# Optimization experiments

Hardware: AMD Instinct MI355X
Metric: run time of the kernel (lower is better)

## Reference

```python
import jax, jax.numpy as jnp
import numpy as np

ALPHA = 0.2  # LeakyReLU negative slope
NEG_INF = -9e15  # matches torch -9000000000000000.0


def setup_inputs() -> dict:
    key = jax.random.key(0)
    k1, k2, k3, k4, k5, k6 = jax.random.split(key, 6)
    N, F_in, F_out = 4096, 512, 256
    adj = jax.random.randint(k1, (N, N), 0, 2, dtype=jnp.int32)
    h = jax.random.normal(k2, (N, F_in), dtype=jnp.float32)
    # proj: Linear(F_in, F_out)
    W = jax.random.normal(k3, (F_in, F_out), dtype=jnp.float32) * (1.0 / np.sqrt(F_in))
    b = jax.random.normal(k4, (F_out,), dtype=jnp.float32) * 0.01
    # proj_a: Linear(2*F_out, 1) split into the two halves acting on src/dst features
    a1 = jax.random.normal(k5, (F_out,), dtype=jnp.float32) * (1.0 / np.sqrt(2 * F_out))
    a2 = jax.random.normal(k6, (F_out,), dtype=jnp.float32) * (1.0 / np.sqrt(2 * F_out))
    a_b = jnp.zeros((), dtype=jnp.float32)
    return {"adj": adj, "h": h, "W": W, "b": b, "a1": a1, "a2": a2, "a_b": a_b}


def reference(adj, h, W, b, a1, a2, a_b):
    # wh = proj(h): [N, F_out]
    wh = h @ W + b
    # Fused form of the N x N x 2F concat + Linear(2F,1):
    # logits[i, j] = wh[i] . a1 + wh[j] . a2 + a_b
    f_src = wh @ a1  # [N]
    f_dst = wh @ a2  # [N]
    e = jax.nn.leaky_relu(f_src[:, None] + f_dst[None, :] + a_b, negative_slope=ALPHA)
    e = jnp.where(adj > 0, e, NEG_INF)
    att = jax.nn.softmax(e, axis=-1)  # F.softmax legacy dim=1 for 2D
    # dropout: inference mode (no-op) for deterministic reference
    out = att @ wh  # [N, F_out]
    return jax.nn.elu(out)  # concat=True
```

## Files before the change

### kernel.cpp

```cpp
#include <hip/hip_runtime.h>

#define NN   4096
#define FIN  512
#define FOUT 256
#define ALPHA 0.2f

typedef __attribute__((ext_vector_type(8))) short short8;
typedef __attribute__((ext_vector_type(4))) float f32x4;
typedef unsigned short u16;
typedef unsigned int u32;
typedef unsigned long long u64;

__device__ __forceinline__ u16 f2bf(float x) {
    union { float f; unsigned u; } v; v.f = x;
    unsigned r = v.u + 0x7FFF + ((v.u >> 16) & 1);
    return (u16)(r >> 16);
}

__global__ __launch_bounds__(256) void k_wt(const float* __restrict__ W,
                                            u16* __restrict__ Wt,
                                            float* __restrict__ fs,
                                            float* __restrict__ fd) {
    __shared__ float s[64 * 65];
    const int t  = threadIdx.x;
    const int g  = (blockIdx.y * gridDim.x + blockIdx.x) * 256 + t;
    if (g < NN) fs[g] = 0.f; else fd[g - NN] = 0.f;
    const int f0 = blockIdx.x * 64;
    const int k0 = blockIdx.y * 64;
    #pragma unroll
    for (int p = 0; p < 4; ++p) {
        int q = t + 256 * p, rr = q >> 4, cc = q & 15;
        float4 w4 = *(const float4*)&W[(size_t)(k0 + rr) * FOUT + f0 + cc * 4];
        s[(cc * 4 + 0) * 65 + rr] = w4.x;
        s[(cc * 4 + 1) * 65 + rr] = w4.y;
        s[(cc * 4 + 2) * 65 + rr] = w4.z;
        s[(cc * 4 + 3) * 65 + rr] = w4.w;
    }
    __syncthreads();
    #pragma unroll
    for (int p = 0; p < 4; ++p) {
        int q = t + 256 * p, f = q >> 4, kg = q & 15;
        ushort4 o;
        o.x = f2bf(s[f * 65 + kg * 4 + 0]);
        o.y = f2bf(s[f * 65 + kg * 4 + 1]);
        o.z = f2bf(s[f * 65 + kg * 4 + 2]);
        o.w = f2bf(s[f * 65 + kg * 4 + 3]);
        *(ushort4*)&Wt[(size_t)(f0 + f) * FIN + k0 + kg * 4] = o;
    }
}

#define HS 520
__global__ __launch_bounds__(256) void k_pb(const float* __restrict__ h,
                                            const u16* __restrict__ Wt,
                                            const float* __restrict__ bias,
                                            const float* __restrict__ a1,
                                            const float* __restrict__ a2,
                                            const int* __restrict__ adj,
                                            u16* __restrict__ whT,
                                            float* __restrict__ fs,
                                            float* __restrict__ fd,
                                            u64* __restrict__ bits) {
    __shared__ u16 s_h[32 * HS];
    const int bid = blockIdx.x;
    const int t   = threadIdx.x;
    if (bid >= 512) {
        const int l = t & 63, wv = t >> 6;
        const int row  = (bid - 512) * 2 + (wv >> 1);
        const int half = wv & 1;
        const size_t base = (size_t)row * NN + half * 2048;
        u64* dst = bits + (size_t)row * 64 + half * 32;
        #pragma unroll
        for (int o = 0; o < 8; ++o) {
            u64 b0 = __ballot(adj[base + (o * 4 + 0) * 64 + l] > 0);
            u64 b1 = __ballot(adj[base + (o * 4 + 1) * 64 + l] > 0);
            u64 b2 = __ballot(adj[base + (o * 4 + 2) * 64 + l] > 0);
            u64 b3 = __ballot(adj[base + (o * 4 + 3) * 64 + l] > 0);
            if (l == 0) {
                dst[o * 4 + 0] = b0;
                dst[o * 4 + 1] = b1;
                dst[o * 4 + 2] = b2;
                dst[o * 4 + 3] = b3;
            }
        }
        return;
    }
    const int f0 = (bid & 3) * 64;
    const int i0 = (bid >> 2) * 32;
    #pragma unroll
    for (int p = 0; p < 16; ++p) {
        int q = t + 256 * p, row = q >> 7, c4 = q & 127;
        float4 v = *(const float4*)&h[(size_t)(i0 + row) * FIN + c4 * 4];
        ushort4 o; o.x = f2bf(v.x); o.y = f2bf(v.y); o.z = f2bf(v.z); o.w = f2bf(v.w);
        *(ushort4*)&s_h[row * HS + c4 * 4] = o;
    }
    __syncthreads();
    const int w = t >> 6, l = t & 63, n = l & 15, quad = l >> 4;
    const int hh = w & 1, fh = w >> 1;
    f32x4 acc[2] = {{0.f,0.f,0.f,0.f},{0.f,0.f,0.f,0.f}};
    #pragma unroll
    for (int k0 = 0; k0 < FIN; k0 += 32) {
        short8 a = *(const short8*)&s_h[(hh * 16 + n) * HS + k0 + quad * 8];
        short8 b0 = *(const short8*)&Wt[(size_t)(f0 + fh * 32 + n) * FIN + k0 + quad * 8];
        short8 b1 = *(const short8*)&Wt[(size_t)(f0 + fh * 32 + 16 + n) * FIN + k0 + quad * 8];
        acc[0] = __builtin_amdgcn_mfma_f32_16x16x32_bf16(a, b0, acc[0], 0, 0, 0);
        acc[1] = __builtin_amdgcn_mfma_f32_16x16x32_bf16(a, b1, acc[1], 0, 0, 0);
    }
    const int fb = f0 + fh * 32 + n;
    const float bv0 = bias[fb],  bv1 = bias[fb + 16];
    const float a10 = a1[fb],    a11 = a1[fb + 16];
    const float a20 = a2[fb],    a21 = a2[fb + 16];
    u16* wt_tile = whT + (size_t)(i0 >> 5) * (FOUT * 32);
    float d1[4], d2[4];
    #pragma unroll
    for (int r = 0; r < 4; ++r) {
        const int ic = hh * 16 + quad * 4 + r;
        const float v0 = acc[0][r] + bv0;
        const float v1 = acc[1][r] + bv1;
        wt_tile[fb * 32 + ic]        = f2bf(v0);
        wt_tile[(fb + 16) * 32 + ic] = f2bf(v1);
        d1[r] = v0 * a10 + v1 * a11;
        d2[r] = v0 * a20 + v1 * a21;
    }
    #pragma unroll
    for (int m = 1; m < 16; m <<= 1) {
        #pragma unroll
        for (int r = 0; r < 4; ++r) {
            d1[r] += __shfl_xor(d1[r], m);
            d2[r] += __shfl_xor(d2[r], m);
        }
    }
    if (n == 0) {
        #pragma unroll
        for (int r = 0; r < 4; ++r) {
            const int i = i0 + hh * 16 + quad * 4 + r;
            atomicAdd(&fs[i], d1[r]);
            atomicAdd(&fd[i], d2[r]);
        }
    }
}

#define BI 32
#define CJ 8

__device__ __forceinline__ void comp_step(
        const short8& b0, const short8& b1, const short8& b2, const short8& b3,
        const float* s_F, const float* s_H, int joff, int jq8,
        u32 w0, u32 w1, float E0, float G0, float E1, float G1,
        f32x4 (&acc)[2][4], float& rs0, float& rs1) {
    const float4 Fa = *(const float4*)&s_F[joff + jq8];
    const float4 Fb = *(const float4*)&s_F[joff + jq8 + 4];
    const float4 Ha = *(const float4*)&s_H[joff + jq8];
    const float4 Hb = *(const float4*)&s_H[joff + jq8 + 4];
    const u32 bw0 = w0 >> jq8, bw1 = w1 >> jq8;
    float q0, q1, q2, q3, q4, q5, q6, q7;
    u32 d0, d1, d2, d3;
    union { short8 v; u32 d[4]; } o0, o1;
#define PEL1(FV, HV, BW, K, E, G, RS, PP) do { \
        float _m = fmaxf((E) * (FV), (G) * (HV)); \
        PP = ((BW) & (1u << (K))) ? _m : 0.f; RS += PP; } while (0)
    PEL1(Fa.x, Ha.x, bw0, 0, E0, G0, rs0, q0);
    PEL1(Fa.y, Ha.y, bw0, 1, E0, G0, rs0, q1);
    PEL1(Fa.z, Ha.z, bw0, 2, E0, G0, rs0, q2);
    PEL1(Fa.w, Ha.w, bw0, 3, E0, G0, rs0, q3);
    PEL1(Fb.x, Hb.x, bw0, 4, E0, G0, rs0, q4);
    PEL1(Fb.y, Hb.y, bw0, 5, E0, G0, rs0, q5);
    PEL1(Fb.z, Hb.z, bw0, 6, E0, G0, rs0, q6);
    PEL1(Fb.w, Hb.w, bw0, 7, E0, G0, rs0, q7);
    asm("v_cvt_pk_bf16_f32 %0, %1, %2" : "=v"(d0) : "v"(q0), "v"(q1));
    asm("v_cvt_pk_bf16_f32 %0, %1, %2" : "=v"(d1) : "v"(q2), "v"(q3));
    asm("v_cvt_pk_bf16_f32 %0, %1, %2" : "=v"(d2) : "v"(q4), "v"(q5));
    asm("v_cvt_pk_bf16_f32 %0, %1, %2" : "=v"(d3) : "v"(q6), "v"(q7));
    o0.d[0] = d0; o0.d[1] = d1; o0.d[2] = d2; o0.d[3] = d3;
    PEL1(Fa.x, Ha.x, bw1, 0, E1, G1, rs1, q0);
    PEL1(Fa.y, Ha.y, bw1, 1, E1, G1, rs1, q1);
    PEL1(Fa.z, Ha.z, bw1, 2, E1, G1, rs1, q2);
    PEL1(Fa.w, Ha.w, bw1, 3, E1, G1, rs1, q3);
    PEL1(Fb.x, Hb.x, bw1, 4, E1, G1, rs1, q4);
    PEL1(Fb.y, Hb.y, bw1, 5, E1, G1, rs1, q5);
    PEL1(Fb.z, Hb.z, bw1, 6, E1, G1, rs1, q6);
    PEL1(Fb.w, Hb.w, bw1, 7, E1, G1, rs1, q7);
#undef PEL1
    asm("v_cvt_pk_bf16_f32 %0, %1, %2" : "=v"(d0) : "v"(q0), "v"(q1));
    asm("v_cvt_pk_bf16_f32 %0, %1, %2" : "=v"(d1) : "v"(q2), "v"(q3));
    asm("v_cvt_pk_bf16_f32 %0, %1, %2" : "=v"(d2) : "v"(q4), "v"(q5));
    asm("v_cvt_pk_bf16_f32 %0, %1, %2" : "=v"(d3) : "v"(q6), "v"(q7));
    o1.d[0] = d0; o1.d[1] = d1; o1.d[2] = d2; o1.d[3] = d3;
    __builtin_amdgcn_s_setprio(1);
    acc[0][0] = __builtin_amdgcn_mfma_f32_16x16x32_bf16(o0.v, b0, acc[0][0], 0, 0, 0);
    acc[0][1] = __builtin_amdgcn_mfma_f32_16x16x32_bf16(o0.v, b1, acc[0][1], 0, 0, 0);
    acc[0][2] = __builtin_amdgcn_mfma_f32_16x16x32_bf16(o0.v, b2, acc[0][2], 0, 0, 0);
    acc[0][3] = __builtin_amdgcn_mfma_f32_16x16x32_bf16(o0.v, b3, acc[0][3], 0, 0, 0);
    acc[1][0] = __builtin_amdgcn_mfma_f32_16x16x32_bf16(o1.v, b0, acc[1][0], 0, 0, 0);
    acc[1][1] = __builtin_amdgcn_mfma_f32_16x16x32_bf16(o1.v, b1, acc[1][1], 0, 0, 0);
    acc[1][2] = __builtin_amdgcn_mfma_f32_16x16x32_bf16(o1.v, b2, acc[1][2], 0, 0, 0);
    acc[1][3] = __builtin_amdgcn_mfma_f32_16x16x32_bf16(o1.v, b3, acc[1][3], 0, 0, 0);
    __builtin_amdgcn_s_setprio(0);
}

__global__ __launch_bounds__(256) void k_attn(const u32* __restrict__ bits,
                                              const u16* __restrict__ whT,
                                              const float* __restrict__ fs,
                                              const float* __restrict__ fd,
                                              const float* __restrict__ ab,
                                              float* __restrict__ part,
                                              float* __restrict__ psum) {
    __shared__ float s_F[NN / CJ], s_H[NN / CJ];
    const int t = threadIdx.x;
    const int w = t >> 6, l = t & 63, n = l & 15, quad = l >> 4;
    const int i0 = blockIdx.x * BI;
    const int c  = blockIdx.y;
    const int jbeg = c * (NN / CJ), jend = jbeg + (NN / CJ);
    const int fw  = w * 64;
    const int jq8 = quad * 8;

    const float abv = ab[0];
    const float s0 = fs[i0 + n] + abv;
    const float s1 = fs[i0 + 16 + n] + abv;
    const float E0 = __expf(s0), G0 = __expf(ALPHA * s0);
    const float E1 = __expf(s1), G1 = __expf(ALPHA * s1);

    const u32* B0 = bits + (size_t)(i0 + n) * 128;
    const u32* B1 = bits + (size_t)(i0 + 16 + n) * 128;
    uint4 m0 = *(const uint4*)&B0[jbeg >> 5];
    uint4 m1 = *(const uint4*)&B1[jbeg >> 5];

    short8 Ab0, Ab1, Ab2, Ab3, Bb0, Bb1, Bb2, Bb3;
#define LDB(P, J0) do { const u16* tb_ = whT + (size_t)((J0) >> 5) * (FOUT * 32) + quad * 8; \
        P##0 = *(const short8*)&tb_[(fw + n) * 32]; \
        P##1 = *(const short8*)&tb_[(fw + n + 16) * 32]; \
        P##2 = *(const short8*)&tb_[(fw + n + 32) * 32]; \
        P##3 = *(const short8*)&tb_[(fw + n + 48) * 32]; } while (0)

    LDB(Ab, jbeg);

    if (t < 128) {
        float4 v = *(const float4*)&fd[jbeg + t * 4];
        float4 F, H;
        F.x = __expf(v.x); F.y = __expf(v.y); F.z = __expf(v.z); F.w = __expf(v.w);
        H.x = __expf(ALPHA * v.x); H.y = __expf(ALPHA * v.y);
        H.z = __expf(ALPHA * v.z); H.w = __expf(ALPHA * v.w);
        *(float4*)&s_F[t * 4] = F;
        *(float4*)&s_H[t * 4] = H;
    }
    __syncthreads();

    f32x4 acc[2][4] = {{{0.f,0.f,0.f,0.f},{0.f,0.f,0.f,0.f},{0.f,0.f,0.f,0.f},{0.f,0.f,0.f,0.f}},
                       {{0.f,0.f,0.f,0.f},{0.f,0.f,0.f,0.f},{0.f,0.f,0.f,0.f},{0.f,0.f,0.f,0.f}}};
    float rs0 = 0.f, rs1 = 0.f;

    #pragma unroll 1
    for (int jb = jbeg; jb < jend; jb += 128) {
        const uint4 cm0 = m0, cm1 = m1;
        if (jb + 128 < jend) {
            m0 = *(const uint4*)&B0[(jb + 128) >> 5];
            m1 = *(const uint4*)&B1[(jb + 128) >> 5];
        }
        LDB(Bb, jb + 32);
        comp_step(Ab0, Ab1, Ab2, Ab3, s_F, s_H, jb - jbeg,      jq8, cm0.x, cm1.x, E0, G0, E1, G1, acc, rs0, rs1);
        LDB(Ab, jb + 64);
        comp_step(Bb0, Bb1, Bb2, Bb3, s_F, s_H, jb - jbeg + 32, jq8, cm0.y, cm1.y, E0, G0, E1, G1, acc, rs0, rs1);
        LDB(Bb, jb + 96);
        comp_step(Ab0, Ab1, Ab2, Ab3, s_F, s_H, jb - jbeg + 64, jq8, cm0.z, cm1.z, E0, G0, E1, G1, acc, rs0, rs1);
        if (jb + 128 < jend) LDB(Ab, jb + 128);
        comp_step(Bb0, Bb1, Bb2, Bb3, s_F, s_H, jb - jbeg + 96, jq8, cm0.w, cm1.w, E0, G0, E1, G1, acc, rs0, rs1);
    }
#undef LDB
    rs0 += __shfl_xor(rs0, 16); rs0 += __shfl_xor(rs0, 32);
    rs1 += __shfl_xor(rs1, 16); rs1 += __shfl_xor(rs1, 32);
    if (w == 0 && quad == 0) {
        psum[(size_t)c * NN + i0 + n]      = rs0;
        psum[(size_t)c * NN + i0 + 16 + n] = rs1;
    }
    float* pc = part + ((size_t)c * NN + i0) * FOUT;
    #pragma unroll
    for (int hf = 0; hf < 2; ++hf)
        #pragma unroll
        for (int u = 0; u < 4; ++u)
            #pragma unroll
            for (int r = 0; r < 4; ++r)
                pc[(size_t)(hf * 16 + quad * 4 + r) * FOUT + fw + u * 16 + n] = acc[hf][u][r];
}

__global__ __launch_bounds__(256) void k_fin(const float* __restrict__ part,
                                             const float* __restrict__ psum,
                                             float* __restrict__ out, int C) {
    const int g = blockIdx.x * 256 + threadIdx.x;
    const int i = g >> 6;
    const size_t s4 = (size_t)NN * FOUT / 4;
    float4 a = ((const float4*)part)[g];
    float s = psum[i];
    for (int c = 1; c < C; ++c) {
        float4 bb = ((const float4*)part)[g + (size_t)c * s4];
        a.x += bb.x; a.y += bb.y; a.z += bb.z; a.w += bb.w;
        s += psum[(size_t)c * NN + i];
    }
    const float inv = 1.0f / s;
    a.x *= inv; a.y *= inv; a.z *= inv; a.w *= inv;
    a.x = a.x > 0.f ? a.x : __expf(a.x) - 1.f;
    a.y = a.y > 0.f ? a.y : __expf(a.y) - 1.f;
    a.z = a.z > 0.f ? a.z : __expf(a.z) - 1.f;
    a.w = a.w > 0.f ? a.w : __expf(a.w) - 1.f;
    ((float4*)out)[g] = a;
}

extern "C" void kernel_launch(void* const* d_in, const int* in_sizes, int n_in,
                              void* d_out, int out_size, void* d_ws, size_t ws_size,
                              hipStream_t stream) {
    const int*   adj = (const int*)  d_in[0];
    const float* h   = (const float*)d_in[1];
    const float* W   = (const float*)d_in[2];
    const float* b   = (const float*)d_in[3];
    const float* a1  = (const float*)d_in[4];
    const float* a2  = (const float*)d_in[5];
    const float* ab  = (const float*)d_in[6];
    float* out = (float*)d_out;

    const int C = CJ;

    float* fs   = (float*)d_ws;
    float* fd   = fs + NN;
    float* psum = fd + NN;
    float* part = psum + (size_t)C * NN;
    u16*   Wt   = (u16*)(part + (size_t)C * NN * FOUT);
    u16*   whT  = Wt + (size_t)FOUT * FIN;
    u64*   bits = (u64*)(whT + (size_t)NN * FOUT);

    k_wt  <<<dim3(FOUT / 64, FIN / 64), 256, 0, stream>>>(W, Wt, fs, fd);
    k_pb  <<<512 + NN / 2, 256, 0, stream>>>(h, Wt, b, a1, a2, adj, whT, fs, fd, bits);
    k_attn<<<dim3(NN / BI, CJ), 256, 0, stream>>>((const u32*)bits, whT, fs, fd, ab, part, psum);
    k_fin <<<(NN * FOUT / 4) / 256, 256, 0, stream>>>(part, psum, out, C);
}
```

Baseline: 154.4 us.

## Retile attention block to 64 rows with 2x2 warp split over rows and features

```diff
diff --git a/kernel.cpp b/kernel.cpp
--- a/kernel.cpp
+++ b/kernel.cpp
@@ -139,14 +139,13 @@
     }
 }
 
-#define BI 32
 #define CJ 8
 
 __device__ __forceinline__ void comp_step(
-        const short8& b0, const short8& b1, const short8& b2, const short8& b3,
+        const short8 (&b)[8],
         const float* s_F, const float* s_H, int joff, int jq8,
         u32 w0, u32 w1, float E0, float G0, float E1, float G1,
-        f32x4 (&acc)[2][4], float& rs0, float& rs1) {
+        f32x4 (&acc)[2][8], float& rs0, float& rs1) {
     const float4 Fa = *(const float4*)&s_F[joff + jq8];
     const float4 Fb = *(const float4*)&s_F[joff + jq8 + 4];
     const float4 Ha = *(const float4*)&s_H[joff + jq8];
@@ -186,52 +185,49 @@
     asm("v_cvt_pk_bf16_f32 %0, %1, %2" : "=v"(d3) : "v"(q6), "v"(q7));
     o1.d[0] = d0; o1.d[1] = d1; o1.d[2] = d2; o1.d[3] = d3;
     __builtin_amdgcn_s_setprio(1);
-    acc[0][0] = __builtin_amdgcn_mfma_f32_16x16x32_bf16(o0.v, b0, acc[0][0], 0, 0, 0);
-    acc[0][1] = __builtin_amdgcn_mfma_f32_16x16x32_bf16(o0.v, b1, acc[0][1], 0, 0, 0);
-    acc[0][2] = __builtin_amdgcn_mfma_f32_16x16x32_bf16(o0.v, b2, acc[0][2], 0, 0, 0);
-    acc[0][3] = __builtin_amdgcn_mfma_f32_16x16x32_bf16(o0.v, b3, acc[0][3], 0, 0, 0);
-    acc[1][0] = __builtin_amdgcn_mfma_f32_16x16x32_bf16(o1.v, b0, acc[1][0], 0, 0, 0);
-    acc[1][1] = __builtin_amdgcn_mfma_f32_16x16x32_bf16(o1.v, b1, acc[1][1], 0, 0, 0);
-    acc[1][2] = __builtin_amdgcn_mfma_f32_16x16x32_bf16(o1.v, b2, acc[1][2], 0, 0, 0);
-    acc[1][3] = __builtin_amdgcn_mfma_f32_16x16x32_bf16(o1.v, b3, acc[1][3], 0, 0, 0);
+    #pragma unroll
+    for (int u = 0; u < 8; ++u) {
+        acc[0][u] = __builtin_amdgcn_mfma_f32_16x16x32_bf16(o0.v, b[u], acc[0][u], 0, 0, 0);
+        acc[1][u] = __builtin_amdgcn_mfma_f32_16x16x32_bf16(o1.v, b[u], acc[1][u], 0, 0, 0);
+    }
     __builtin_amdgcn_s_setprio(0);
 }
 
-__global__ __launch_bounds__(256) void k_attn(const u32* __restrict__ bits,
-                                              const u16* __restrict__ whT,
-                                              const float* __restrict__ fs,
-                                              const float* __restrict__ fd,
-                                              const float* __restrict__ ab,
-                                              float* __restrict__ part,
-                                              float* __restrict__ psum) {
+__global__ __launch_bounds__(256, 2) void k_attn(const u32* __restrict__ bits,
+                                                 const u16* __restrict__ whT,
+                                                 const float* __restrict__ fs,
+                                                 const float* __restrict__ fd,
+                                                 const float* __restrict__ ab,
+                                                 float* __restrict__ part,
+                                                 float* __restrict__ psum) {
     __shared__ float s_F[NN / CJ], s_H[NN / CJ];
     const int t = threadIdx.x;
     const int w = t >> 6, l = t & 63, n = l & 15, quad = l >> 4;
-    const int i0 = blockIdx.x * BI;
+    const int gi0 = blockIdx.x * 64;
+    const int ib  = gi0 + (w & 1) * 32;
+    const int fwb = (w >> 1) * 128;
     const int c  = blockIdx.y;
     const int jbeg = c * (NN / CJ), jend = jbeg + (NN / CJ);
-    const int fw  = w * 64;
     const int jq8 = quad * 8;
 
     const float abv = ab[0];
-    const float s0 = fs[i0 + n] + abv;
-    const float s1 = fs[i0 + 16 + n] + abv;
+    const float s0 = fs[ib + n] + abv;
+    const float s1 = fs[ib + 16 + n] + abv;
     const float E0 = __expf(s0), G0 = __expf(ALPHA * s0);
     const float E1 = __expf(s1), G1 = __expf(ALPHA * s1);
 
-    const u32* B0 = bits + (size_t)(i0 + n) * 128;
-    const u32* B1 = bits + (size_t)(i0 + 16 + n) * 128;
+    const u32* B0 = bits + (size_t)(ib + n) * 128;
+    const u32* B1 = bits + (size_t)(ib + 16 + n) * 128;
     uint4 m0 = *(const uint4*)&B0[jbeg >> 5];
     uint4 m1 = *(const uint4*)&B1[jbeg >> 5];
 
-    short8 Ab0, Ab1, Ab2, Ab3, Bb0, Bb1, Bb2, Bb3;
+    short8 Ba[8], Bb[8];
 #define LDB(P, J0) do { const u16* tb_ = whT + (size_t)((J0) >> 5) * (FOUT * 32) + quad * 8; \
-        P##0 = *(const short8*)&tb_[(fw + n) * 32]; \
-        P##1 = *(const short8*)&tb_[(fw + n + 16) * 32]; \
-        P##2 = *(const short8*)&tb_[(fw + n + 32) * 32]; \
-        P##3 = *(const short8*)&tb_[(fw + n + 48) * 32]; } while (0)
-
-    LDB(Ab, jbeg);
+        _Pragma("unroll") \
+        for (int u = 0; u < 8; ++u) \
+            P[u] = *(const short8*)&tb_[(fwb + u * 16 + n) * 32]; } while (0)
+
+    LDB(Ba, jbeg);
 
     if (t < 128) {
         float4 v = *(const float4*)&fd[jbeg + t * 4];
@@ -244,8 +240,10 @@
     }
     __syncthreads();
 
-    f32x4 acc[2][4] = {{{0.f,0.f,0.f,0.f},{0.f,0.f,0.f,0.f},{0.f,0.f,0.f,0.f},{0.f,0.f,0.f,0.f}},
-                       {{0.f,0.f,0.f,0.f},{0.f,0.f,0.f,0.f},{0.f,0.f,0.f,0.f},{0.f,0.f,0.f,0.f}}};
+    f32x4 acc[2][8] = {{{0.f,0.f,0.f,0.f},{0.f,0.f,0.f,0.f},{0.f,0.f,0.f,0.f},{0.f,0.f,0.f,0.f},
+                        {0.f,0.f,0.f,0.f},{0.f,0.f,0.f,0.f},{0.f,0.f,0.f,0.f},{0.f,0.f,0.f,0.f}},
+                       {{0.f,0.f,0.f,0.f},{0.f,0.f,0.f,0.f},{0.f,0.f,0.f,0.f},{0.f,0.f,0.f,0.f},
+                        {0.f,0.f,0.f,0.f},{0.f,0.f,0.f,0.f},{0.f,0.f,0.f,0.f},{0.f,0.f,0.f,0.f}}};
     float rs0 = 0.f, rs1 = 0.f;
 
     #pragma unroll 1
@@ -256,29 +254,29 @@
             m1 = *(const uint4*)&B1[(jb + 128) >> 5];
         }
         LDB(Bb, jb + 32);
-        comp_step(Ab0, Ab1, Ab2, Ab3, s_F, s_H, jb - jbeg,      jq8, cm0.x, cm1.x, E0, G0, E1, G1, acc, rs0, rs1);
-        LDB(Ab, jb + 64);
-        comp_step(Bb0, Bb1, Bb2, Bb3, s_F, s_H, jb - jbeg + 32, jq8, cm0.y, cm1.y, E0, G0, E1, G1, acc, rs0, rs1);
+        comp_step(Ba, s_F, s_H, jb - jbeg,      jq8, cm0.x, cm1.x, E0, G0, E1, G1, acc, rs0, rs1);
+        LDB(Ba, jb + 64);
+        comp_step(Bb, s_F, s_H, jb - jbeg + 32, jq8, cm0.y, cm1.y, E0, G0, E1, G1, acc, rs0, rs1);
         LDB(Bb, jb + 96);
-        comp_step(Ab0, Ab1, Ab2, Ab3, s_F, s_H, jb - jbeg + 64, jq8, cm0.z, cm1.z, E0, G0, E1, G1, acc, rs0, rs1);
-        if (jb + 128 < jend) LDB(Ab, jb + 128);
-        comp_step(Bb0, Bb1, Bb2, Bb3, s_F, s_H, jb - jbeg + 96, jq8, cm0.w, cm1.w, E0, G0, E1, G1, acc, rs0, rs1);
+        comp_step(Ba, s_F, s_H, jb - jbeg + 64, jq8, cm0.z, cm1.z, E0, G0, E1, G1, acc, rs0, rs1);
+        if (jb + 128 < jend) LDB(Ba, jb + 128);
+        comp_step(Bb, s_F, s_H, jb - jbeg + 96, jq8, cm0.w, cm1.w, E0, G0, E1, G1, acc, rs0, rs1);
     }
 #undef LDB
     rs0 += __shfl_xor(rs0, 16); rs0 += __shfl_xor(rs0, 32);
     rs1 += __shfl_xor(rs1, 16); rs1 += __shfl_xor(rs1, 32);
-    if (w == 0 && quad == 0) {
-        psum[(size_t)c * NN + i0 + n]      = rs0;
-        psum[(size_t)c * NN + i0 + 16 + n] = rs1;
-    }
-    float* pc = part + ((size_t)c * NN + i0) * FOUT;
+    if (w < 2 && quad == 0) {
+        psum[(size_t)c * NN + ib + n]      = rs0;
+        psum[(size_t)c * NN + ib + 16 + n] = rs1;
+    }
+    float* pc = part + ((size_t)c * NN + ib) * FOUT;
     #pragma unroll
     for (int hf = 0; hf < 2; ++hf)
         #pragma unroll
-        for (int u = 0; u < 4; ++u)
+        for (int u = 0; u < 8; ++u)
             #pragma unroll
             for (int r = 0; r < 4; ++r)
-                pc[(size_t)(hf * 16 + quad * 4 + r) * FOUT + fw + u * 16 + n] = acc[hf][u][r];
+                pc[(size_t)(hf * 16 + quad * 4 + r) * FOUT + fwb + u * 16 + n] = acc[hf][u][r];
 }
 
 __global__ __launch_bounds__(256) void k_fin(const float* __restrict__ part,
@@ -327,6 +325,6 @@
 
     k_wt  <<<dim3(FOUT / 64, FIN / 64), 256, 0, stream>>>(W, Wt, fs, fd);
     k_pb  <<<512 + NN / 2, 256, 0, stream>>>(h, Wt, b, a1, a2, adj, whT, fs, fd, bits);
-    k_attn<<<dim3(NN / BI, CJ), 256, 0, stream>>>((const u32*)bits, whT, fs, fd, ab, part, psum);
+    k_attn<<<dim3(NN / 64, CJ), 256, 0, stream>>>((const u32*)bits, whT, fs, fd, ab, part, psum);
     k_fin <<<(NN * FOUT / 4) / 256, 256, 0, stream>>>(part, psum, out, C);
 }
```

Measured after the change: 161.4 us. 4.5% more time.
